# Performance work log

Measured on AMD Instinct MI355X. Metric: run time of the kernel, lower is better.

## Reference

```python
import jax, jax.numpy as jnp
import numpy as np

N_NODES = 20000
N_EDGES = 320000
IN_CH = 256
HID_CH = 256   # 2 * out_channels
OUT_CH = 128


def gcn_conv(x, edge_index, W, b, n_nodes):
    """PyG GCNConv: linear transform, add self-loops, sym-normalized scatter-add."""
    x = x @ W  # [N, C_out]
    loop = jnp.arange(n_nodes, dtype=edge_index.dtype)
    row = jnp.concatenate([edge_index[0], loop])  # source nodes
    col = jnp.concatenate([edge_index[1], loop])  # destination nodes
    deg = jax.ops.segment_sum(jnp.ones_like(col, dtype=x.dtype), col,
                              num_segments=n_nodes)
    deg_inv_sqrt = jnp.where(deg > 0, jax.lax.rsqrt(deg), 0.0)
    norm = deg_inv_sqrt[row] * deg_inv_sqrt[col]  # [E+N]
    msg = x[row] * norm[:, None]                  # gather + scale
    out = jax.ops.segment_sum(msg, col, num_segments=n_nodes)  # scatter-add
    return out + b


def setup_inputs() -> dict:
    key = jax.random.key(0)
    k1, k2, k3, k4, k5 = jax.random.split(key, 5)
    doc_embeds = jax.random.normal(k1, (N_NODES, IN_CH), dtype=jnp.float32)
    edge_index = jax.random.randint(k2, (2, N_EDGES), 0, N_NODES, dtype=jnp.int64)
    # Glorot-style init for GCN weights, zero bias (PyG defaults)
    s1 = 1.0 / np.sqrt(IN_CH)
    s2 = 1.0 / np.sqrt(HID_CH)
    W1 = jax.random.uniform(k3, (IN_CH, HID_CH), jnp.float32, -s1, s1)
    b1 = jnp.zeros((HID_CH,), jnp.float32)
    W2 = jax.random.uniform(k4, (HID_CH, OUT_CH), jnp.float32, -s2, s2)
    b2 = jnp.zeros((OUT_CH,), jnp.float32)
    return {"doc_embeds": doc_embeds, "edge_index": edge_index,
            "W1": W1, "b1": b1, "W2": W2, "b2": b2}


def reference(doc_embeds, edge_index, W1, b1, W2, b2):
    n = doc_embeds.shape[0]
    x = jax.nn.relu(gcn_conv(doc_embeds, edge_index, W1, b1, n))
    x = gcn_conv(x, edge_index, W2, b2, n)
    return x
```

## Files before the change

### kernel.cpp

```cpp
#include <hip/hip_runtime.h>
#include <math.h>

#define N_NODES 20000
#define N_EDGES 320000
#define IN_CH   256
#define HID_CH  256
#define OUT_CH  128
#define CAP     64

typedef __attribute__((ext_vector_type(8))) short short8;
typedef __attribute__((ext_vector_type(8))) unsigned short ushort8;
typedef __attribute__((ext_vector_type(4))) unsigned short ushort4v;
typedef __attribute__((ext_vector_type(4))) float floatx4;
typedef __attribute__((ext_vector_type(2))) float floatx2;
typedef __attribute__((ext_vector_type(4))) _Float16 half4;
typedef __attribute__((ext_vector_type(2))) _Float16 half2v;
typedef __attribute__((ext_vector_type(8))) _Float16 half8;

static __device__ __forceinline__ unsigned short f2bf(float f) {
    unsigned int u = __float_as_uint(f);
    u += 0x7FFFu + ((u >> 16) & 1u);
    return (unsigned short)(u >> 16);
}
static __device__ __forceinline__ float bf2f(unsigned short h) {
    return __uint_as_float(((unsigned int)h) << 16);
}

__global__ __launch_bounds__(256)
void prep_kernel(const float* __restrict__ W1, const float* __restrict__ W2,
                 unsigned short* __restrict__ W1thi, unsigned short* __restrict__ W1tlo,
                 unsigned short* __restrict__ W2thi, unsigned short* __restrict__ W2tlo,
                 const int* __restrict__ row, const int* __restrict__ col,
                 int* __restrict__ deg, unsigned short* __restrict__ srcs) {
    const int g = blockIdx.x * blockDim.x + threadIdx.x;
    const int gsz = gridDim.x * blockDim.x;
    for (int t = g; t < (IN_CH * HID_CH) / 16; t += gsz) {
        int n = t >> 4;
        int kc = (t & 15) * 16;
        ushort8 h0, l0, h1, l1;
#pragma unroll
        for (int j = 0; j < 8; ++j) {
            float x = W1[(size_t)(kc + j) * HID_CH + n];
            h0[j] = f2bf(x); l0[j] = f2bf(x - bf2f(h0[j]));
            float y = W1[(size_t)(kc + 8 + j) * HID_CH + n];
            h1[j] = f2bf(y); l1[j] = f2bf(y - bf2f(h1[j]));
        }
        *(ushort8*)(W1thi + (size_t)n * IN_CH + kc)     = h0;
        *(ushort8*)(W1thi + (size_t)n * IN_CH + kc + 8) = h1;
        *(ushort8*)(W1tlo + (size_t)n * IN_CH + kc)     = l0;
        *(ushort8*)(W1tlo + (size_t)n * IN_CH + kc + 8) = l1;
    }
    for (int t = g; t < (HID_CH * OUT_CH) / 16; t += gsz) {
        int n = t >> 4;
        int kc = (t & 15) * 16;
        ushort8 h0, l0, h1, l1;
#pragma unroll
        for (int j = 0; j < 8; ++j) {
            float x = W2[(size_t)(kc + j) * OUT_CH + n];
            h0[j] = f2bf(x); l0[j] = f2bf(x - bf2f(h0[j]));
            float y = W2[(size_t)(kc + 8 + j) * OUT_CH + n];
            h1[j] = f2bf(y); l1[j] = f2bf(y - bf2f(h1[j]));
        }
        *(ushort8*)(W2thi + (size_t)n * HID_CH + kc)     = h0;
        *(ushort8*)(W2thi + (size_t)n * HID_CH + kc + 8) = h1;
        *(ushort8*)(W2tlo + (size_t)n * HID_CH + kc)     = l0;
        *(ushort8*)(W2tlo + (size_t)n * HID_CH + kc + 8) = l1;
    }
    for (int i = g; i < N_EDGES; i += gsz) {
        int c = col[i];
        int r = row[i];
        int p = atomicAdd(&deg[c], 1);
        srcs[(size_t)c * CAP + p] = (unsigned short)r;
    }
}

#define GK 256
template <int AMODE, int TM>
__global__ __launch_bounds__(256)
void gemm_mfma_kernel(const float* __restrict__ Afp, const _Float16* __restrict__ Ah,
                      const unsigned short* __restrict__ Bthi, const unsigned short* __restrict__ Btlo,
                      const int* __restrict__ deg, _Float16* __restrict__ C, int M, int N) {
    constexpr int MI = TM / 32;
    __shared__ unsigned short As[2][TM][36];
    __shared__ unsigned short Bs[2][128][36];
    const int tid = threadIdx.x;
    const int m0 = blockIdx.y * TM;
    const int n0 = blockIdx.x * 128;
    const int lane = tid & 63;
    const int wave = tid >> 6;
    const int wr = (wave >> 1) * (TM / 2);
    const int wc = (wave & 1) * 64;
    const int lm = lane & 15;
    const int lk = (lane >> 4) * 8;

    floatx4 acc[MI][4];
#pragma unroll
    for (int i = 0; i < MI; ++i)
#pragma unroll
        for (int j = 0; j < 4; ++j) acc[i][j] = (floatx4){0.f, 0.f, 0.f, 0.f};

    for (int k0 = 0; k0 < GK; k0 += 32) {
#pragma unroll
        for (int c = 0; c < TM / 64; ++c) {
            int ch = tid + c * 256;
            int r = ch >> 2;
            int ko = (ch & 3) * 8;
            ushort8 vh = {}, vl = {};
            if (m0 + r < M) {
                float xs[8];
                if (AMODE == 1) {
                    const float* ap = Afp + (size_t)(m0 + r) * GK + k0 + ko;
                    float4 f0 = *(const float4*)ap;
                    float4 f1 = *(const float4*)(ap + 4);
                    xs[0] = f0.x; xs[1] = f0.y; xs[2] = f0.z; xs[3] = f0.w;
                    xs[4] = f1.x; xs[5] = f1.y; xs[6] = f1.z; xs[7] = f1.w;
                } else {
                    half8 hv = *(const half8*)(Ah + (size_t)(m0 + r) * GK + k0 + ko);
#pragma unroll
                    for (int j = 0; j < 8; ++j) xs[j] = (float)hv[j];
                }
#pragma unroll
                for (int j = 0; j < 8; ++j) {
                    vh[j] = f2bf(xs[j]);
                    vl[j] = f2bf(xs[j] - bf2f(vh[j]));
                }
            }
            *(ushort8*)&As[0][r][ko] = vh;
            *(ushort8*)&As[1][r][ko] = vl;
        }
#pragma unroll
        for (int c = 0; c < 2; ++c) {
            int ch = tid + c * 256;
            int r = ch >> 2;
            int ko = (ch & 3) * 8;
            size_t gb = (size_t)(n0 + r) * GK + k0 + ko;
            *(ushort8*)&Bs[0][r][ko] = *(const ushort8*)(Bthi + gb);
            *(ushort8*)&Bs[1][r][ko] = *(const ushort8*)(Btlo + gb);
        }
        __syncthreads();

        short8 ah[MI], al[MI], bh[4], bl[4];
#pragma unroll
        for (int i = 0; i < MI; ++i) {
            ah[i] = *(const short8*)&As[0][wr + i * 16 + lm][lk];
            al[i] = *(const short8*)&As[1][wr + i * 16 + lm][lk];
        }
#pragma unroll
        for (int j = 0; j < 4; ++j) {
            bh[j] = *(const short8*)&Bs[0][wc + j * 16 + lm][lk];
            bl[j] = *(const short8*)&Bs[1][wc + j * 16 + lm][lk];
        }
#pragma unroll
        for (int i = 0; i < MI; ++i)
#pragma unroll
            for (int j = 0; j < 4; ++j) {
                acc[i][j] = __builtin_amdgcn_mfma_f32_16x16x32_bf16(ah[i], bh[j], acc[i][j], 0, 0, 0);
                acc[i][j] = __builtin_amdgcn_mfma_f32_16x16x32_bf16(ah[i], bl[j], acc[i][j], 0, 0, 0);
                acc[i][j] = __builtin_amdgcn_mfma_f32_16x16x32_bf16(al[i], bh[j], acc[i][j], 0, 0, 0);
            }
        __syncthreads();
    }

#pragma unroll
    for (int i = 0; i < MI; ++i) {
#pragma unroll
        for (int r = 0; r < 4; ++r) {
            int rowi = m0 + wr + i * 16 + (lane >> 4) * 4 + r;
            if (rowi < M) {
                float dr = 1.0f / sqrtf((float)(deg[rowi] + 1));
#pragma unroll
                for (int j = 0; j < 4; ++j) {
                    C[(size_t)rowi * N + n0 + wc + j * 16 + lm] = (_Float16)(dr * acc[i][j][r]);
                }
            }
        }
    }
}

template <int C, int NSLICE, int MODE>
__global__ __launch_bounds__(256)
void gather_sliced_kernel(const _Float16* __restrict__ X, const int* __restrict__ deg,
                          const unsigned short* __restrict__ srcs,
                          const float* __restrict__ bias, float* __restrict__ outf,
                          _Float16* __restrict__ outh, int n) {
    constexpr int SW = C / NSLICE;
    static_assert(SW == 32, "slice must be 32 channels");
    const int slice = blockIdx.x % NSLICE;
    const int ngrp  = blockIdx.x / NSLICE;
    const int wave = threadIdx.x >> 6;
    const int lane = threadIdx.x & 63;
    const int g  = lane >> 4;
    const int sl = lane & 15;
    const int node = ngrp * 16 + wave * 4 + g;
    if (node >= n) return;
    const int choff = slice * SW + sl * 2;
    const size_t beg = (size_t)node * CAP;
    const int cnt = deg[node];

    float a0 = 0.f, a1 = 0.f;
    int e = 0;
    for (; e + 4 <= cnt; e += 4) {
        ushort4v s4 = *(const ushort4v*)(srcs + beg + e);
        half2v v0 = *(const half2v*)(X + (size_t)s4.x * C + choff);
        half2v v1 = *(const half2v*)(X + (size_t)s4.y * C + choff);
        half2v v2 = *(const half2v*)(X + (size_t)s4.z * C + choff);
        half2v v3 = *(const half2v*)(X + (size_t)s4.w * C + choff);
        a0 += (float)v0.x + (float)v1.x + (float)v2.x + (float)v3.x;
        a1 += (float)v0.y + (float)v1.y + (float)v2.y + (float)v3.y;
    }
    for (; e < cnt; ++e) {
        int r = srcs[beg + e];
        half2v v = *(const half2v*)(X + (size_t)r * C + choff);
        a0 += (float)v.x; a1 += (float)v.y;
    }

    const float dc = 1.0f / sqrtf((float)(cnt + 1));
    half2v vsh = *(const half2v*)(X + (size_t)node * C + choff);
    float2 bb = *(const float2*)(bias + choff);

    float o0 = dc * (a0 + (float)vsh.x) + bb.x;
    float o1 = dc * (a1 + (float)vsh.y) + bb.y;

    if constexpr (MODE == 1) {
        half2v h;
        h.x = (_Float16)fmaxf(o0, 0.f);
        h.y = (_Float16)fmaxf(o1, 0.f);
        *(half2v*)(outh + (size_t)node * C + choff) = h;
    } else {
        floatx2 o = {o0, o1};
        __builtin_nontemporal_store(o, (floatx2*)(outf + (size_t)node * C + choff));
    }
}

extern "C" void kernel_launch(void* const* d_in, const int* in_sizes, int n_in,
                              void* d_out, int out_size, void* d_ws, size_t ws_size,
                              hipStream_t stream) {
    const float* doc_embeds = (const float*)d_in[0];
    const int*   edge_index = (const int*)d_in[1];
    const float* W1 = (const float*)d_in[2];
    const float* b1 = (const float*)d_in[3];
    const float* W2 = (const float*)d_in[4];
    const float* b2 = (const float*)d_in[5];
    float* out = (float*)d_out;

    const int* row = edge_index;
    const int* col = edge_index + N_EDGES;

    char* ws = (char*)d_ws;
    auto align_up = [](size_t x) { return (x + 255) / 256 * 256; };

    _Float16* X1s = (_Float16*)(ws);
    _Float16* H1  = (_Float16*)(ws + align_up((size_t)N_NODES * HID_CH * 2));
    _Float16* X2s = X1s;
    char* meta = (char*)(ws + 2 * align_up((size_t)N_NODES * HID_CH * 2));
    unsigned short* W1thi = (unsigned short*)(meta); meta += align_up((size_t)IN_CH * HID_CH * 2);
    unsigned short* W1tlo = (unsigned short*)(meta); meta += align_up((size_t)IN_CH * HID_CH * 2);
    unsigned short* W2thi = (unsigned short*)(meta); meta += align_up((size_t)HID_CH * OUT_CH * 2);
    unsigned short* W2tlo = (unsigned short*)(meta); meta += align_up((size_t)HID_CH * OUT_CH * 2);
    int*            deg   = (int*)(meta);            meta += align_up((size_t)N_NODES * 4);
    unsigned short* srcs  = (unsigned short*)(meta);

    hipMemsetAsync(deg, 0, (size_t)N_NODES * 4, stream);
    prep_kernel<<<(N_EDGES + 255) / 256, 256, 0, stream>>>(
        W1, W2, W1thi, W1tlo, W2thi, W2tlo, row, col, deg, srcs);

    {
        dim3 grid(HID_CH / 128, (N_NODES + 63) / 64);
        gemm_mfma_kernel<1, 64><<<grid, 256, 0, stream>>>(
            doc_embeds, nullptr, W1thi, W1tlo, deg, X1s, N_NODES, HID_CH);
    }
    gather_sliced_kernel<HID_CH, 8, 1><<<((N_NODES + 15) / 16) * 8, 256, 0, stream>>>(
        X1s, deg, srcs, b1, nullptr, H1, N_NODES);

    {
        dim3 grid(OUT_CH / 128, (N_NODES + 63) / 64);
        gemm_mfma_kernel<2, 64><<<grid, 256, 0, stream>>>(
            nullptr, H1, W2thi, W2tlo, deg, X2s, N_NODES, OUT_CH);
    }
    gather_sliced_kernel<OUT_CH, 4, 0><<<((N_NODES + 15) / 16) * 4, 256, 0, stream>>>(
        X2s, deg, srcs, b2, out, nullptr, N_NODES);
}
```

Measured before the change: 174.5 us.

## Fuse GCN pipeline into one cooperative persistent kernel with grid syncs

Replaces the five separate launches (prep, two GEMMs, two gathers) with a single cooperative kernel of 512 persistent blocks that run each stage in turn, separated by grid-wide syncs. It also pre-splits the input embeddings into bf16 hi/lo planes during the prep phase, and has the first gather write H1 as bf16 hi/lo instead of fp16, so the GEMM A-tile loads become plain copies. This removes launch gaps and the per-tile conversion work. In exchange it adds extra traffic for the hi/lo buffers, costs grid-sync barriers, and fixes the grid at 512 blocks, which may underuse the GPU or fail to be co-resident.

```diff
diff --git a/kernel.cpp b/kernel.cpp
--- a/kernel.cpp
+++ b/kernel.cpp
@@ -1,5 +1,8 @@
 #include <hip/hip_runtime.h>
+#include <hip/hip_cooperative_groups.h>
 #include <math.h>
+
+namespace cg = cooperative_groups;
 
 #define N_NODES 20000
 #define N_EDGES 320000
@@ -7,15 +10,17 @@
 #define HID_CH  256
 #define OUT_CH  128
 #define CAP     64
+#define GK      256
+#define NBLK    512
+#define NTHR    256
 
 typedef __attribute__((ext_vector_type(8))) short short8;
 typedef __attribute__((ext_vector_type(8))) unsigned short ushort8;
 typedef __attribute__((ext_vector_type(4))) unsigned short ushort4v;
+typedef __attribute__((ext_vector_type(2))) unsigned short ushort2v;
 typedef __attribute__((ext_vector_type(4))) float floatx4;
 typedef __attribute__((ext_vector_type(2))) float floatx2;
-typedef __attribute__((ext_vector_type(4))) _Float16 half4;
 typedef __attribute__((ext_vector_type(2))) _Float16 half2v;
-typedef __attribute__((ext_vector_type(8))) _Float16 half8;
 
 static __device__ __forceinline__ unsigned short f2bf(float f) {
     unsigned int u = __float_as_uint(f);
@@ -26,122 +31,67 @@
     return __uint_as_float(((unsigned int)h) << 16);
 }
 
-__global__ __launch_bounds__(256)
-void prep_kernel(const float* __restrict__ W1, const float* __restrict__ W2,
-                 unsigned short* __restrict__ W1thi, unsigned short* __restrict__ W1tlo,
-                 unsigned short* __restrict__ W2thi, unsigned short* __restrict__ W2tlo,
-                 const int* __restrict__ row, const int* __restrict__ col,
-                 int* __restrict__ deg, unsigned short* __restrict__ srcs) {
-    const int g = blockIdx.x * blockDim.x + threadIdx.x;
-    const int gsz = gridDim.x * blockDim.x;
-    for (int t = g; t < (IN_CH * HID_CH) / 16; t += gsz) {
-        int n = t >> 4;
-        int kc = (t & 15) * 16;
-        ushort8 h0, l0, h1, l1;
-#pragma unroll
-        for (int j = 0; j < 8; ++j) {
-            float x = W1[(size_t)(kc + j) * HID_CH + n];
-            h0[j] = f2bf(x); l0[j] = f2bf(x - bf2f(h0[j]));
-            float y = W1[(size_t)(kc + 8 + j) * HID_CH + n];
-            h1[j] = f2bf(y); l1[j] = f2bf(y - bf2f(h1[j]));
-        }
-        *(ushort8*)(W1thi + (size_t)n * IN_CH + kc)     = h0;
-        *(ushort8*)(W1thi + (size_t)n * IN_CH + kc + 8) = h1;
-        *(ushort8*)(W1tlo + (size_t)n * IN_CH + kc)     = l0;
-        *(ushort8*)(W1tlo + (size_t)n * IN_CH + kc + 8) = l1;
-    }
-    for (int t = g; t < (HID_CH * OUT_CH) / 16; t += gsz) {
-        int n = t >> 4;
-        int kc = (t & 15) * 16;
-        ushort8 h0, l0, h1, l1;
-#pragma unroll
-        for (int j = 0; j < 8; ++j) {
-            float x = W2[(size_t)(kc + j) * OUT_CH + n];
-            h0[j] = f2bf(x); l0[j] = f2bf(x - bf2f(h0[j]));
-            float y = W2[(size_t)(kc + 8 + j) * OUT_CH + n];
-            h1[j] = f2bf(y); l1[j] = f2bf(y - bf2f(h1[j]));
-        }
-        *(ushort8*)(W2thi + (size_t)n * HID_CH + kc)     = h0;
-        *(ushort8*)(W2thi + (size_t)n * HID_CH + kc + 8) = h1;
-        *(ushort8*)(W2tlo + (size_t)n * HID_CH + kc)     = l0;
-        *(ushort8*)(W2tlo + (size_t)n * HID_CH + kc + 8) = l1;
-    }
-    for (int i = g; i < N_EDGES; i += gsz) {
-        int c = col[i];
-        int r = row[i];
-        int p = atomicAdd(&deg[c], 1);
-        srcs[(size_t)c * CAP + p] = (unsigned short)r;
-    }
-}
-
-#define GK 256
-template <int AMODE, int TM>
-__global__ __launch_bounds__(256)
-void gemm_mfma_kernel(const float* __restrict__ Afp, const _Float16* __restrict__ Ah,
-                      const unsigned short* __restrict__ Bthi, const unsigned short* __restrict__ Btlo,
-                      const int* __restrict__ deg, _Float16* __restrict__ C, int M, int N) {
-    constexpr int MI = TM / 32;
-    __shared__ unsigned short As[2][TM][36];
-    __shared__ unsigned short Bs[2][128][36];
-    const int tid = threadIdx.x;
-    const int m0 = blockIdx.y * TM;
-    const int n0 = blockIdx.x * 128;
+struct Params {
+    const float* doc; const int* row; const int* col;
+    const float* W1; const float* b1; const float* W2; const float* b2;
+    unsigned short* Ehi; unsigned short* Elo;
+    unsigned short* W1thi; unsigned short* W1tlo;
+    unsigned short* W2thi; unsigned short* W2tlo;
+    int* deg; unsigned short* srcs;
+    _Float16* X1s;
+    unsigned short* H1hi; unsigned short* H1lo;
+    float* out;
+};
+
+static __device__ __forceinline__ void gemm_tile(
+    const unsigned short* __restrict__ Ahi, const unsigned short* __restrict__ Alo,
+    const unsigned short* __restrict__ Bhi, const unsigned short* __restrict__ Blo,
+    const int* __restrict__ deg, _Float16* __restrict__ Cc,
+    int M, int N, int m0, int n0,
+    unsigned short (&As)[2][64][36], unsigned short (&Bs)[2][128][36])
+{
+    const int tid  = threadIdx.x;
     const int lane = tid & 63;
     const int wave = tid >> 6;
-    const int wr = (wave >> 1) * (TM / 2);
+    const int wr = (wave >> 1) * 32;
     const int wc = (wave & 1) * 64;
     const int lm = lane & 15;
     const int lk = (lane >> 4) * 8;
 
-    floatx4 acc[MI][4];
-#pragma unroll
-    for (int i = 0; i < MI; ++i)
+    floatx4 acc[2][4];
+#pragma unroll
+    for (int i = 0; i < 2; ++i)
 #pragma unroll
         for (int j = 0; j < 4; ++j) acc[i][j] = (floatx4){0.f, 0.f, 0.f, 0.f};
 
+    const int ar  = tid >> 2;
+    const int ako = (tid & 3) * 8;
+
     for (int k0 = 0; k0 < GK; k0 += 32) {
-#pragma unroll
-        for (int c = 0; c < TM / 64; ++c) {
-            int ch = tid + c * 256;
-            int r = ch >> 2;
-            int ko = (ch & 3) * 8;
+        {
             ushort8 vh = {}, vl = {};
-            if (m0 + r < M) {
-                float xs[8];
-                if (AMODE == 1) {
-                    const float* ap = Afp + (size_t)(m0 + r) * GK + k0 + ko;
-                    float4 f0 = *(const float4*)ap;
-                    float4 f1 = *(const float4*)(ap + 4);
-                    xs[0] = f0.x; xs[1] = f0.y; xs[2] = f0.z; xs[3] = f0.w;
-                    xs[4] = f1.x; xs[5] = f1.y; xs[6] = f1.z; xs[7] = f1.w;
-                } else {
-                    half8 hv = *(const half8*)(Ah + (size_t)(m0 + r) * GK + k0 + ko);
-#pragma unroll
-                    for (int j = 0; j < 8; ++j) xs[j] = (float)hv[j];
-                }
-#pragma unroll
-                for (int j = 0; j < 8; ++j) {
-                    vh[j] = f2bf(xs[j]);
-                    vl[j] = f2bf(xs[j] - bf2f(vh[j]));
-                }
+            if (m0 + ar < M) {
+                size_t ga = (size_t)(m0 + ar) * GK + k0 + ako;
+                vh = *(const ushort8*)(Ahi + ga);
+                vl = *(const ushort8*)(Alo + ga);
             }
-            *(ushort8*)&As[0][r][ko] = vh;
-            *(ushort8*)&As[1][r][ko] = vl;
+            *(ushort8*)&As[0][ar][ako] = vh;
+            *(ushort8*)&As[1][ar][ako] = vl;
         }
 #pragma unroll
         for (int c = 0; c < 2; ++c) {
-            int ch = tid + c * 256;
-            int r = ch >> 2;
+            int ch = tid + c * NTHR;
+            int r  = ch >> 2;
             int ko = (ch & 3) * 8;
             size_t gb = (size_t)(n0 + r) * GK + k0 + ko;
-            *(ushort8*)&Bs[0][r][ko] = *(const ushort8*)(Bthi + gb);
-            *(ushort8*)&Bs[1][r][ko] = *(const ushort8*)(Btlo + gb);
+            *(ushort8*)&Bs[0][r][ko] = *(const ushort8*)(Bhi + gb);
+            *(ushort8*)&Bs[1][r][ko] = *(const ushort8*)(Blo + gb);
         }
         __syncthreads();
 
-        short8 ah[MI], al[MI], bh[4], bl[4];
-#pragma unroll
-        for (int i = 0; i < MI; ++i) {
+        short8 ah[2], al[2], bh[4], bl[4];
+#pragma unroll
+        for (int i = 0; i < 2; ++i) {
             ah[i] = *(const short8*)&As[0][wr + i * 16 + lm][lk];
             al[i] = *(const short8*)&As[1][wr + i * 16 + lm][lk];
         }
@@ -151,7 +101,7 @@
             bl[j] = *(const short8*)&Bs[1][wc + j * 16 + lm][lk];
         }
 #pragma unroll
-        for (int i = 0; i < MI; ++i)
+        for (int i = 0; i < 2; ++i)
 #pragma unroll
             for (int j = 0; j < 4; ++j) {
                 acc[i][j] = __builtin_amdgcn_mfma_f32_16x16x32_bf16(ah[i], bh[j], acc[i][j], 0, 0, 0);
@@ -162,7 +112,7 @@
     }
 
 #pragma unroll
-    for (int i = 0; i < MI; ++i) {
+    for (int i = 0; i < 2; ++i) {
 #pragma unroll
         for (int r = 0; r < 4; ++r) {
             int rowi = m0 + wr + i * 16 + (lane >> 4) * 4 + r;
@@ -170,28 +120,29 @@
                 float dr = 1.0f / sqrtf((float)(deg[rowi] + 1));
 #pragma unroll
                 for (int j = 0; j < 4; ++j) {
-                    C[(size_t)rowi * N + n0 + wc + j * 16 + lm] = (_Float16)(dr * acc[i][j][r]);
+                    Cc[(size_t)rowi * N + n0 + wc + j * 16 + lm] = (_Float16)(dr * acc[i][j][r]);
                 }
             }
         }
     }
 }
 
-template <int C, int NSLICE, int MODE>
-__global__ __launch_bounds__(256)
-void gather_sliced_kernel(const _Float16* __restrict__ X, const int* __restrict__ deg,
-                          const unsigned short* __restrict__ srcs,
-                          const float* __restrict__ bias, float* __restrict__ outf,
-                          _Float16* __restrict__ outh, int n) {
-    constexpr int SW = C / NSLICE;
+template <int CC, int NSLICE, int MODE>
+static __device__ __forceinline__ void gather_tile(
+    const _Float16* __restrict__ X, const int* __restrict__ deg,
+    const unsigned short* __restrict__ srcs, const float* __restrict__ bias,
+    float* __restrict__ outf, unsigned short* __restrict__ outhi,
+    unsigned short* __restrict__ outlo, int n, int vblk)
+{
+    constexpr int SW = CC / NSLICE;
     static_assert(SW == 32, "slice must be 32 channels");
-    const int slice = blockIdx.x % NSLICE;
-    const int ngrp  = blockIdx.x / NSLICE;
+    const int slice = vblk % NSLICE;
+    const int ngrp  = vblk / NSLICE;
     const int wave = threadIdx.x >> 6;
     const int lane = threadIdx.x & 63;
-    const int g  = lane >> 4;
+    const int gg = lane >> 4;
     const int sl = lane & 15;
-    const int node = ngrp * 16 + wave * 4 + g;
+    const int node = ngrp * 16 + wave * 4 + gg;
     if (node >= n) return;
     const int choff = slice * SW + sl * 2;
     const size_t beg = (size_t)node * CAP;
@@ -201,82 +152,162 @@
     int e = 0;
     for (; e + 4 <= cnt; e += 4) {
         ushort4v s4 = *(const ushort4v*)(srcs + beg + e);
-        half2v v0 = *(const half2v*)(X + (size_t)s4.x * C + choff);
-        half2v v1 = *(const half2v*)(X + (size_t)s4.y * C + choff);
-        half2v v2 = *(const half2v*)(X + (size_t)s4.z * C + choff);
-        half2v v3 = *(const half2v*)(X + (size_t)s4.w * C + choff);
+        half2v v0 = *(const half2v*)(X + (size_t)s4.x * CC + choff);
+        half2v v1 = *(const half2v*)(X + (size_t)s4.y * CC + choff);
+        half2v v2 = *(const half2v*)(X + (size_t)s4.z * CC + choff);
+        half2v v3 = *(const half2v*)(X + (size_t)s4.w * CC + choff);
         a0 += (float)v0.x + (float)v1.x + (float)v2.x + (float)v3.x;
         a1 += (float)v0.y + (float)v1.y + (float)v2.y + (float)v3.y;
     }
     for (; e < cnt; ++e) {
         int r = srcs[beg + e];
-        half2v v = *(const half2v*)(X + (size_t)r * C + choff);
+        half2v v = *(const half2v*)(X + (size_t)r * CC + choff);
         a0 += (float)v.x; a1 += (float)v.y;
     }
 
     const float dc = 1.0f / sqrtf((float)(cnt + 1));
-    half2v vsh = *(const half2v*)(X + (size_t)node * C + choff);
+    half2v vsh = *(const half2v*)(X + (size_t)node * CC + choff);
     float2 bb = *(const float2*)(bias + choff);
 
     float o0 = dc * (a0 + (float)vsh.x) + bb.x;
     float o1 = dc * (a1 + (float)vsh.y) + bb.y;
 
     if constexpr (MODE == 1) {
-        half2v h;
-        h.x = (_Float16)fmaxf(o0, 0.f);
-        h.y = (_Float16)fmaxf(o1, 0.f);
-        *(half2v*)(outh + (size_t)node * C + choff) = h;
+        float r0 = fmaxf(o0, 0.f), r1 = fmaxf(o1, 0.f);
+        ushort2v hv, lv;
+        hv.x = f2bf(r0); lv.x = f2bf(r0 - bf2f(hv.x));
+        hv.y = f2bf(r1); lv.y = f2bf(r1 - bf2f(hv.y));
+        *(ushort2v*)(outhi + (size_t)node * CC + choff) = hv;
+        *(ushort2v*)(outlo + (size_t)node * CC + choff) = lv;
     } else {
         floatx2 o = {o0, o1};
-        __builtin_nontemporal_store(o, (floatx2*)(outf + (size_t)node * C + choff));
-    }
+        __builtin_nontemporal_store(o, (floatx2*)(outf + (size_t)node * CC + choff));
+    }
+}
+
+__global__ __launch_bounds__(NTHR, 2)
+void fused_gcn(Params p)
+{
+    __shared__ unsigned short As[2][64][36];
+    __shared__ unsigned short Bs[2][128][36];
+    cg::grid_group gridg = cg::this_grid();
+    const int tid = threadIdx.x;
+    const int bid = blockIdx.x;
+    const int g   = bid * NTHR + tid;
+    const int gsz = NBLK * NTHR;
+
+    for (int t = g; t < (IN_CH * HID_CH) / 16; t += gsz) {
+        int n = t >> 4;
+        int kc = (t & 15) * 16;
+        ushort8 h0, l0, h1, l1;
+#pragma unroll
+        for (int j = 0; j < 8; ++j) {
+            float x = p.W1[(size_t)(kc + j) * HID_CH + n];
+            h0[j] = f2bf(x); l0[j] = f2bf(x - bf2f(h0[j]));
+            float y = p.W1[(size_t)(kc + 8 + j) * HID_CH + n];
+            h1[j] = f2bf(y); l1[j] = f2bf(y - bf2f(h1[j]));
+        }
+        *(ushort8*)(p.W1thi + (size_t)n * IN_CH + kc)     = h0;
+        *(ushort8*)(p.W1thi + (size_t)n * IN_CH + kc + 8) = h1;
+        *(ushort8*)(p.W1tlo + (size_t)n * IN_CH + kc)     = l0;
+        *(ushort8*)(p.W1tlo + (size_t)n * IN_CH + kc + 8) = l1;
+    }
+    for (int t = g; t < (HID_CH * OUT_CH) / 16; t += gsz) {
+        int n = t >> 4;
+        int kc = (t & 15) * 16;
+        ushort8 h0, l0, h1, l1;
+#pragma unroll
+        for (int j = 0; j < 8; ++j) {
+            float x = p.W2[(size_t)(kc + j) * OUT_CH + n];
+            h0[j] = f2bf(x); l0[j] = f2bf(x - bf2f(h0[j]));
+            float y = p.W2[(size_t)(kc + 8 + j) * OUT_CH + n];
+            h1[j] = f2bf(y); l1[j] = f2bf(y - bf2f(h1[j]));
+        }
+        *(ushort8*)(p.W2thi + (size_t)n * HID_CH + kc)     = h0;
+        *(ushort8*)(p.W2thi + (size_t)n * HID_CH + kc + 8) = h1;
+        *(ushort8*)(p.W2tlo + (size_t)n * HID_CH + kc)     = l0;
+        *(ushort8*)(p.W2tlo + (size_t)n * HID_CH + kc + 8) = l1;
+    }
+    for (int t = g; t < (N_NODES * IN_CH) / 16; t += gsz) {
+        int node = t >> 4;
+        int kc = (t & 15) * 16;
+        const float* ap = p.doc + (size_t)node * IN_CH + kc;
+        float4 f0 = *(const float4*)(ap);
+        float4 f1 = *(const float4*)(ap + 4);
+        float4 f2 = *(const float4*)(ap + 8);
+        float4 f3 = *(const float4*)(ap + 12);
+        float xs[16] = {f0.x, f0.y, f0.z, f0.w, f1.x, f1.y, f1.z, f1.w,
+                        f2.x, f2.y, f2.z, f2.w, f3.x, f3.y, f3.z, f3.w};
+        ushort8 h0, l0, h1, l1;
+#pragma unroll
+        for (int j = 0; j < 8; ++j) {
+            h0[j] = f2bf(xs[j]);     l0[j] = f2bf(xs[j] - bf2f(h0[j]));
+            h1[j] = f2bf(xs[8 + j]); l1[j] = f2bf(xs[8 + j] - bf2f(h1[j]));
+        }
+        *(ushort8*)(p.Ehi + (size_t)node * IN_CH + kc)     = h0;
+        *(ushort8*)(p.Ehi + (size_t)node * IN_CH + kc + 8) = h1;
+        *(ushort8*)(p.Elo + (size_t)node * IN_CH + kc)     = l0;
+        *(ushort8*)(p.Elo + (size_t)node * IN_CH + kc + 8) = l1;
+    }
+    for (int i = g; i < N_EDGES; i += gsz) {
+        int c = p.col[i];
+        int r = p.row[i];
+        int q = atomicAdd(&p.deg[c], 1);
+        p.srcs[(size_t)c * CAP + q] = (unsigned short)r;
+    }
+    gridg.sync();
+
+    for (int tile = bid; tile < 2 * ((N_NODES + 63) / 64); tile += NBLK)
+        gemm_tile(p.Ehi, p.Elo, p.W1thi, p.W1tlo, p.deg, p.X1s,
+                  N_NODES, HID_CH, (tile >> 1) * 64, (tile & 1) * 128, As, Bs);
+    gridg.sync();
+
+    for (int v = bid; v < ((N_NODES + 15) / 16) * 8; v += NBLK)
+        gather_tile<HID_CH, 8, 1>(p.X1s, p.deg, p.srcs, p.b1,
+                                  nullptr, p.H1hi, p.H1lo, N_NODES, v);
+    gridg.sync();
+
+    for (int tile = bid; tile < (N_NODES + 63) / 64; tile += NBLK)
+        gemm_tile(p.H1hi, p.H1lo, p.W2thi, p.W2tlo, p.deg, p.X1s,
+                  N_NODES, OUT_CH, tile * 64, 0, As, Bs);
+    gridg.sync();
+
+    for (int v = bid; v < ((N_NODES + 15) / 16) * 4; v += NBLK)
+        gather_tile<OUT_CH, 4, 0>(p.X1s, p.deg, p.srcs, p.b2,
+                                  p.out, nullptr, nullptr, N_NODES, v);
 }
 
 extern "C" void kernel_launch(void* const* d_in, const int* in_sizes, int n_in,
                               void* d_out, int out_size, void* d_ws, size_t ws_size,
-                              hipStream_t stream) {
-    const float* doc_embeds = (const float*)d_in[0];
-    const int*   edge_index = (const int*)d_in[1];
-    const float* W1 = (const float*)d_in[2];
-    const float* b1 = (const float*)d_in[3];
-    const float* W2 = (const float*)d_in[4];
-    const float* b2 = (const float*)d_in[5];
-    float* out = (float*)d_out;
-
-    const int* row = edge_index;
-    const int* col = edge_index + N_EDGES;
+                              hipStream_t stream)
+{
+    Params p;
+    p.doc = (const float*)d_in[0];
+    const int* ei = (const int*)d_in[1];
+    p.row = ei;
+    p.col = ei + N_EDGES;
+    p.W1 = (const float*)d_in[2];
+    p.b1 = (const float*)d_in[3];
+    p.W2 = (const float*)d_in[4];
+    p.b2 = (const float*)d_in[5];
+    p.out = (float*)d_out;
 
     char* ws = (char*)d_ws;
-    auto align_up = [](size_t x) { return (x + 255) / 256 * 256; };
-
-    _Float16* X1s = (_Float16*)(ws);
-    _Float16* H1  = (_Float16*)(ws + align_up((size_t)N_NODES * HID_CH * 2));
-    _Float16* X2s = X1s;
-    char* meta = (char*)(ws + 2 * align_up((size_t)N_NODES * HID_CH * 2));
-    unsigned short* W1thi = (unsigned short*)(meta); meta += align_up((size_t)IN_CH * HID_CH * 2);
-    unsigned short* W1tlo = (unsigned short*)(meta); meta += align_up((size_t)IN_CH * HID_CH * 2);
-    unsigned short* W2thi = (unsigned short*)(meta); meta += align_up((size_t)HID_CH * OUT_CH * 2);
-    unsigned short* W2tlo = (unsigned short*)(meta); meta += align_up((size_t)HID_CH * OUT_CH * 2);
-    int*            deg   = (int*)(meta);            meta += align_up((size_t)N_NODES * 4);
-    unsigned short* srcs  = (unsigned short*)(meta);
-
-    hipMemsetAsync(deg, 0, (size_t)N_NODES * 4, stream);
-    prep_kernel<<<(N_EDGES + 255) / 256, 256, 0, stream>>>(
-        W1, W2, W1thi, W1tlo, W2thi, W2tlo, row, col, deg, srcs);
-
-    {
-        dim3 grid(HID_CH / 128, (N_NODES + 63) / 64);
-        gemm_mfma_kernel<1, 64><<<grid, 256, 0, stream>>>(
-            doc_embeds, nullptr, W1thi, W1tlo, deg, X1s, N_NODES, HID_CH);
-    }
-    gather_sliced_kernel<HID_CH, 8, 1><<<((N_NODES + 15) / 16) * 8, 256, 0, stream>>>(
-        X1s, deg, srcs, b1, nullptr, H1, N_NODES);
-
-    {
-        dim3 grid(OUT_CH / 128, (N_NODES + 63) / 64);
-        gemm_mfma_kernel<2, 64><<<grid, 256, 0, stream>>>(
-            nullptr, H1, W2thi, W2tlo, deg, X2s, N_NODES, OUT_CH);
-    }
-    gather_sliced_kernel<OUT_CH, 4, 0><<<((N_NODES + 15) / 16) * 4, 256, 0, stream>>>(
-        X2s, deg, srcs, b2, out, nullptr, N_NODES);
-}
+    auto au = [](size_t x) { return (x + 255) / 256 * 256; };
+    p.X1s   = (_Float16*)ws;       ws += au((size_t)N_NODES * HID_CH * 2);
+    p.Ehi   = (unsigned short*)ws; ws += au((size_t)N_NODES * IN_CH * 2);
+    p.Elo   = (unsigned short*)ws; ws += au((size_t)N_NODES * IN_CH * 2);
+    p.H1hi  = (unsigned short*)ws; ws += au((size_t)N_NODES * HID_CH * 2);
+    p.H1lo  = (unsigned short*)ws; ws += au((size_t)N_NODES * HID_CH * 2);
+    p.W1thi = (unsigned short*)ws; ws += au((size_t)IN_CH * HID_CH * 2);
+    p.W1tlo = (unsigned short*)ws; ws += au((size_t)IN_CH * HID_CH * 2);
+    p.W2thi = (unsigned short*)ws; ws += au((size_t)HID_CH * OUT_CH * 2);
+    p.W2tlo = (unsigned short*)ws; ws += au((size_t)HID_CH * OUT_CH * 2);
+    p.deg   = (int*)ws;            ws += au((size_t)N_NODES * 4);
+    p.srcs  = (unsigned short*)ws;
+
+    hipMemsetAsync(p.deg, 0, (size_t)N_NODES * 4, stream);
+    void* args[] = { &p };
+    hipLaunchCooperativeKernel((const void*)fused_gcn, dim3(NBLK), dim3(NTHR),
+                               args, 0, stream);
+}
```

Result: slower. 552.2 us (+216.4%).
